# Kernel optimization log

Measured on AMD Instinct MI355X. Metric: run time of the kernel, lower is better.

## Reference

```python
import jax, jax.numpy as jnp
import numpy as np

B, T, C = 16, 1024, 512
K = 25          # decomp kernel_size
NW = 4          # num_wavelets
SEQ_LEN = T
EPS = 1e-5


def causal_ma(x, k):
    # causal moving average over time with replicate left-pad; x: [B,T,C]
    xp = jnp.pad(x, ((0, 0), (k - 1, 0), (0, 0)), mode='edge')
    cs = jnp.cumsum(xp, axis=1)
    cs0 = jnp.concatenate([jnp.zeros_like(cs[:, :1]), cs], axis=1)
    return (cs0[:, k:] - cs0[:, :-k]) / k


def dwconv3(x, w, b):
    # depthwise conv1d, kernel 3, replicate padding; x: [B,T,C], w: [C,3], b: [C]
    xp = jnp.pad(x, ((0, 0), (1, 1), (0, 0)), mode='edge')
    return xp[:, :-2] * w[:, 0] + xp[:, 1:-1] * w[:, 1] + xp[:, 2:] * w[:, 2] + b


def setup_inputs() -> dict:
    key = jax.random.key(0)
    ks = jax.random.split(key, 12)
    s = 0.02
    return {
        'x': jax.random.normal(ks[0], (B, T, C), dtype=jnp.float32),
        'trend_conv_w': jax.random.normal(ks[1], (C, 3), jnp.float32) * s,
        'trend_conv_b': jnp.zeros((C,), jnp.float32),
        'spike_conv_w': jax.random.normal(ks[2], (C, 3), jnp.float32) * s,
        'spike_conv_b': jnp.zeros((C,), jnp.float32),
        'slope_conv_w': jax.random.normal(ks[3], (C, 3), jnp.float32) * s,
        'slope_conv_b': jnp.zeros((C,), jnp.float32),
        'cheby_coeffs': jax.random.normal(ks[4], (C, C, 4), jnp.float32) * (1.0 / np.sqrt(C * 4)),
        'hyper_w1': jax.random.normal(ks[5], (2 * C, C), jnp.float32) * s,
        'hyper_b1': jnp.zeros((C,), jnp.float32),
        'hyper_w2': jax.random.normal(ks[6], (C, NW * 2), jnp.float32) * s,
        'hyper_b2': jnp.zeros((NW * 2,), jnp.float32),
        'amp_w': jax.random.normal(ks[7], (C, C), jnp.float32) * s,
        'amp_b': jnp.zeros((C,), jnp.float32),
        'wavelet_w': jax.random.normal(ks[8], (NW, C, C), jnp.float32) * (1.0 / np.sqrt(C)),
        'ln_gamma': jnp.ones((C,), jnp.float32),
        'ln_beta': jnp.zeros((C,), jnp.float32),
    }


def reference(x, trend_conv_w, trend_conv_b, spike_conv_w, spike_conv_b,
              slope_conv_w, slope_conv_b, cheby_coeffs,
              hyper_w1, hyper_b1, hyper_w2, hyper_b2,
              amp_w, amp_b, wavelet_w, ln_gamma, ln_beta):
    # --- causal frequency decomposition ---
    trend_part = causal_ma(x, K)              # [B,T,C]
    spike_part = x - trend_part

    # --- depthwise local convs ---
    trend_ctx = dwconv3(trend_part, trend_conv_w, trend_conv_b)
    spike_ctx = dwconv3(spike_part, spike_conv_w, spike_conv_b)

    # --- ChebyKAN on trend (degree 3) ---
    xt = jnp.tanh(trend_ctx)
    basis = jnp.stack([jnp.ones_like(xt), xt, 2 * xt * xt - 1,
                       xt * (4 * xt * xt - 3)], axis=-1)      # [B,T,C,4]
    trend_out = jnp.einsum('btcd,cod->bto', basis, cheby_coeffs)

    # --- hypernetwork for wavelet params ---
    slope = dwconv3(trend_part, slope_conv_w, slope_conv_b)
    slope_pool = slope.mean(axis=1)            # mean over time -> [B,C]
    value_pool = trend_part.mean(axis=1)       # [B,C]
    h = jnp.concatenate([slope_pool, value_pool], axis=-1)
    h = jax.nn.silu(h @ hyper_w1 + hyper_b1)
    params = (h @ hyper_w2 + hyper_b2).reshape(-1, 1, NW, 2)
    dyn_a = jax.nn.softplus(params[..., 0]) + 0.01          # [B,1,NW]
    dyn_b = jax.nn.sigmoid(params[..., 1]) * SEQ_LEN        # [B,1,NW]

    # --- adaptive wavelet KAN on spike ---
    pos = jnp.arange(T, dtype=x.dtype)[None, :, None]       # [1,T,1]
    z = (pos - dyn_b) / dyn_a                               # [B,T,NW]
    psi = (1.0 - z * z) * jnp.exp(-0.5 * z * z)             # Ricker wavelet
    spike_out = jnp.einsum('btw,btc,wco->bto', psi, spike_ctx, wavelet_w)

    # --- amplitude gate, residual, LayerNorm (dropout = identity in eval) ---
    amp_scale = jax.nn.sigmoid(trend_out @ amp_w + amp_b) * 2.0
    out = trend_out + spike_out * amp_scale
    y = out + x
    mu = y.mean(axis=-1, keepdims=True)
    var = ((y - mu) ** 2).mean(axis=-1, keepdims=True)
    return (y - mu) * jax.lax.rsqrt(var + EPS) * ln_gamma + ln_beta
```

## Files before the change

### kernel.cpp

```cpp
#include <hip/hip_runtime.h>
#include <hip/hip_bf16.h>
#include <math.h>

typedef __hip_bfloat16 bf16;
typedef __attribute__((ext_vector_type(8))) short s8v;
typedef __attribute__((ext_vector_type(4))) float f4v;

#define B_   16
#define T_   1024
#define C_   512
#define M_   (B_*T_)
#define NW_  4
#define KWIN 25
#define TCHUNK 16
#define NCHUNK (T_/TCHUNK)

__device__ __forceinline__ float b2f(bf16 v){ return __bfloat162float(v); }
__device__ __forceinline__ bf16  f2b(float v){ return __float2bfloat16(v); }

__device__ __forceinline__ float ftanh(float x){
    float e = __expf(2.f * x);
    return 1.f - 2.f * __builtin_amdgcn_rcpf(e + 1.f);
}
__device__ __forceinline__ float fsig(float x){
    return __builtin_amdgcn_rcpf(1.f + __expf(-x));
}

__device__ __forceinline__ void gload16(const bf16* g, bf16* l) {
    __builtin_amdgcn_global_load_lds(
        (const __attribute__((address_space(1))) void*)g,
        (__attribute__((address_space(3))) void*)l, 16, 0, 0);
}

__global__ __launch_bounds__(256) void repack_t_kernel(
    const float* __restrict__ wav, const float* __restrict__ ampw,
    bf16* __restrict__ WWT, bf16* __restrict__ AWT)
{
    __shared__ float tile[32][33];
    const int z = blockIdx.z;
    const int ct = blockIdx.x * 32, ot = blockIdx.y * 32;
    const int tx = threadIdx.x & 31, ty = threadIdx.x >> 5;
    const float* src = (z < 4) ? wav + (size_t)z * 262144 : ampw;
    #pragma unroll
    for (int r = 0; r < 32; r += 8)
        tile[ty + r][tx] = src[(size_t)(ct + ty + r) * 512 + ot + tx];
    __syncthreads();
    #pragma unroll
    for (int r = 0; r < 32; r += 8) {
        int o = ot + ty + r, c = ct + tx;
        bf16 v = f2b(tile[tx][ty + r]);
        if (z < 4) WWT[(size_t)o * 2048 + z * 512 + c] = v;
        else       AWT[(size_t)o * 512 + c] = v;
    }
}

__global__ __launch_bounds__(256) void repack_cct_kernel(
    const float* __restrict__ cheby,
    bf16* __restrict__ CCT)
{
    __shared__ float t1[32][33], t2[32][33], t3[32][33];
    const int ct = blockIdx.x * 32, ot = blockIdx.y * 32;
    const int tx = threadIdx.x & 31, ty = threadIdx.x >> 5;
    #pragma unroll
    for (int r = 0; r < 32; r += 8) {
        float4 w = *(const float4*)&cheby[(size_t)(ct + ty + r) * 2048 + (size_t)(ot + tx) * 4];
        t1[ty + r][tx] = w.y - 3.f * w.w;
        t2[ty + r][tx] = 2.f * w.z;
        t3[ty + r][tx] = 4.f * w.w;
    }
    __syncthreads();
    #pragma unroll
    for (int r = 0; r < 32; r += 8) {
        int o = ot + ty + r, c = ct + tx;
        size_t base = (size_t)o * 1536 + c;
        CCT[base]        = f2b(t1[tx][ty + r]);
        CCT[base + 512]  = f2b(t2[tx][ty + r]);
        CCT[base + 1024] = f2b(t3[tx][ty + r]);
    }
}

__global__ __launch_bounds__(256) void bias0_kernel(
    const float* __restrict__ cheby, float* __restrict__ bias0)
{
    __shared__ float red[8][33];
    const int tx = threadIdx.x & 31, ty = threadIdx.x >> 5;
    const int o = blockIdx.x * 32 + tx;
    float s = 0.f;
    for (int c = ty; c < 512; c += 8) {
        const float* p = &cheby[(size_t)c * 2048 + (size_t)o * 4];
        s += p[0] - p[2];
    }
    red[ty][tx] = s;
    __syncthreads();
    if (ty == 0) {
        float t = 0.f;
        #pragma unroll
        for (int q = 0; q < 8; ++q) t += red[q][tx];
        bias0[o] = t;
    }
}

__global__ __launch_bounds__(256) void transpose_w1_kernel(
    const float* __restrict__ w1, float* __restrict__ w1t)
{
    __shared__ float tile[32][33];
    const int bo = blockIdx.x, bj = blockIdx.y;
    const int tx = threadIdx.x & 31, ty = threadIdx.x >> 5;
    #pragma unroll
    for (int r = 0; r < 32; r += 8)
        tile[ty + r][tx] = w1[(size_t)(bj * 32 + ty + r) * 512 + bo * 32 + tx];
    __syncthreads();
    #pragma unroll
    for (int r = 0; r < 32; r += 8)
        w1t[(size_t)(bo * 32 + ty + r) * 1024 + bj * 32 + tx] = tile[tx][ty + r];
}

__global__ __launch_bounds__(256) void decomp_kernel(
    const float* __restrict__ x,
    const float* __restrict__ tcw, const float* __restrict__ tcb,
    const float* __restrict__ scw, const float* __restrict__ scb,
    const float* __restrict__ lcw, const float* __restrict__ lcb,
    bf16* __restrict__ xt,
    bf16* __restrict__ sctx,
    float* __restrict__ slope_part, float* __restrict__ value_part)
{
    const int c     = threadIdx.x * 2;
    const int chunk = blockIdx.x;
    const int b     = blockIdx.y;
    const int t0    = chunk * TCHUNK;
    const float* xb = x + (size_t)b * T_ * C_ + c;

    float w0t[2], w1t_[2], w2t[2], bt[2], w0s[2], w1s[2], w2s[2], bs[2], w0l[2], w1l[2], w2l[2], bl[2];
    #pragma unroll
    for (int e = 0; e < 2; ++e) {
        w0t[e]=tcw[(c+e)*3+0]; w1t_[e]=tcw[(c+e)*3+1]; w2t[e]=tcw[(c+e)*3+2]; bt[e]=tcb[c+e];
        w0s[e]=scw[(c+e)*3+0]; w1s[e]=scw[(c+e)*3+1]; w2s[e]=scw[(c+e)*3+2]; bs[e]=scb[c+e];
        w0l[e]=lcw[(c+e)*3+0]; w1l[e]=lcw[(c+e)*3+1]; w2l[e]=lcw[(c+e)*3+2]; bl[e]=lcb[c+e];
    }

    const float inv = 1.f / KWIN;
    float S0 = 0.f, S1 = 0.f;
    float trm[2], tr0[2], xm[2], x0v[2], sAcc[2] = {0.f,0.f}, vAcc[2] = {0.f,0.f};

    auto BODY = [&](int t, float2 an, float2 dn, bool adv) {
        float trp[2], xp[2];
        if (adv) {
            S0 += an.x - dn.x; S1 += an.y - dn.y;
            trp[0] = S0 * inv; trp[1] = S1 * inv;
            xp[0] = an.x; xp[1] = an.y;
        } else {
            trp[0] = tr0[0]; trp[1] = tr0[1];
            xp[0] = x0v[0];  xp[1] = x0v[1];
        }
        union { bf16 h[2]; unsigned u; } u1, usc;
        #pragma unroll
        for (int e = 0; e < 2; ++e) {
            float tctx = w0t[e]*trm[e] + w1t_[e]*tr0[e] + w2t[e]*trp[e] + bt[e];
            float sm = xm[e]-trm[e], s0 = x0v[e]-tr0[e], sp = xp[e]-trp[e];
            float sv = w0s[e]*sm + w1s[e]*s0 + w2s[e]*sp + bs[e];
            float sl = w0l[e]*trm[e] + w1l[e]*tr0[e] + w2l[e]*trp[e] + bl[e];
            sAcc[e] += sl; vAcc[e] += tr0[e];
            u1.h[e] = f2b(ftanh(tctx)); usc.h[e] = f2b(sv);
            trm[e] = tr0[e]; tr0[e] = trp[e]; xm[e] = x0v[e]; x0v[e] = xp[e];
        }
        size_t m = (size_t)b * T_ + t;
        *(unsigned*)&xt[m * C_ + c]   = u1.u;
        *(unsigned*)&sctx[m * C_ + c] = usc.u;
    };

    if (chunk >= 2 && chunk <= NCHUNK - 2) {
        const float* p = xb + (size_t)(t0 - KWIN) * C_;
        #pragma unroll
        for (int i = 0; i < KWIN; ++i) {
            float2 v = *(const float2*)(p + (size_t)i * C_);
            S0 += v.x; S1 += v.y;
        }
        trm[0] = S0 * inv; trm[1] = S1 * inv;
        float2 a = *(const float2*)(p + (size_t)KWIN * C_);
        float2 d = *(const float2*)p;
        S0 += a.x - d.x; S1 += a.y - d.y;
        tr0[0] = S0 * inv; tr0[1] = S1 * inv;
        float2 vm = *(const float2*)(p + (size_t)(KWIN - 1) * C_);
        xm[0] = vm.x; xm[1] = vm.y;
        x0v[0] = a.x; x0v[1] = a.y;

        #pragma unroll
        for (int tt = 0; tt < TCHUNK; ++tt) {
            float2 an = *(const float2*)(p + (size_t)(KWIN + 1 + tt) * C_);
            float2 dn = *(const float2*)(p + (size_t)(1 + tt) * C_);
            BODY(t0 + tt, an, dn, true);
        }
    } else {
        auto X = [&](int i) -> float2 {
            i = i < 0 ? 0 : (i > T_ - 1 ? T_ - 1 : i);
            return *(const float2*)&xb[(size_t)i * C_];
        };
        int j0 = (t0 > 0) ? (t0 - 1) : 0;
        #pragma unroll
        for (int i = j0 - (KWIN - 1); i <= j0; ++i) { float2 v = X(i); S0 += v.x; S1 += v.y; }
        trm[0] = S0 * inv; trm[1] = S1 * inv;
        if (t0 > 0) {
            float2 a = X(t0), d = X(t0 - KWIN);
            S0 += a.x - d.x; S1 += a.y - d.y;
            tr0[0] = S0 * inv; tr0[1] = S1 * inv;
        } else { tr0[0] = trm[0]; tr0[1] = trm[1]; }
        { float2 v = X(t0 - 1); xm[0] = v.x; xm[1] = v.y; }
        { float2 v = X(t0);     x0v[0] = v.x; x0v[1] = v.y; }

        #pragma unroll
        for (int tt = 0; tt < TCHUNK; ++tt) {
            int t = t0 + tt, tn = t + 1;
            bool adv = (tn <= T_ - 1);
            float2 an = make_float2(0.f, 0.f), dn = make_float2(0.f, 0.f);
            if (adv) { an = X(tn); dn = X(tn - KWIN); }
            BODY(t, an, dn, adv);
        }
    }
    int pidx = (chunk * B_ + b) * C_ + c;
    *(float2*)&slope_part[pidx] = make_float2(sAcc[0], sAcc[1]);
    *(float2*)&value_part[pidx] = make_float2(vAcc[0], vAcc[1]);
}

__global__ __launch_bounds__(256) void pool_kernel(
    const float* __restrict__ slope_part, const float* __restrict__ value_part,
    float* __restrict__ pc)
{
    int idx = blockIdx.x * 256 + threadIdx.x;
    int b = idx >> 10, j = idx & 1023;
    int c = j & 511;
    const float* src = (j < 512) ? slope_part : value_part;
    float s = 0.f;
    #pragma unroll 8
    for (int ch = 0; ch < NCHUNK; ++ch) s += src[(ch * B_ + b) * C_ + c];
    pc[idx] = s * (1.f / T_);
}

__global__ __launch_bounds__(256) void hyper1_kernel(
    const float* __restrict__ pc, const float* __restrict__ w1t,
    const float* __restrict__ b1, float* __restrict__ h)
{
    const int o = blockIdx.x, t = threadIdx.x;
    const float4 w = *(const float4*)&w1t[(size_t)o * 1024 + t * 4];
    float acc[16];
    #pragma unroll
    for (int b = 0; b < 16; ++b) {
        float4 p = *(const float4*)&pc[(size_t)b * 1024 + t * 4];
        acc[b] = w.x * p.x + w.y * p.y + w.z * p.z + w.w * p.w;
    }
    #pragma unroll
    for (int off = 32; off >= 1; off >>= 1)
        #pragma unroll
        for (int b = 0; b < 16; ++b) acc[b] += __shfl_down(acc[b], off);
    __shared__ float red[4][16];
    int lane = t & 63, wv = t >> 6;
    if (lane == 0)
        #pragma unroll
        for (int b = 0; b < 16; ++b) red[wv][b] = acc[b];
    __syncthreads();
    if (t < 16) {
        float s = red[0][t] + red[1][t] + red[2][t] + red[3][t] + b1[o];
        h[(size_t)t * 512 + o] = s / (1.f + expf(-s));
    }
}

__global__ __launch_bounds__(128) void hyper2_kernel(
    const float* __restrict__ h, const float* __restrict__ w2,
    const float* __restrict__ b2, float* __restrict__ dyn_a, float* __restrict__ dyn_b)
{
    __shared__ float pp[16][8];
    const int t = threadIdx.x, b = t >> 3, o = t & 7;
    float acc = b2[o];
    #pragma unroll 4
    for (int j = 0; j < 512; ++j) acc += h[(size_t)b * 512 + j] * w2[j * 8 + o];
    pp[b][o] = acc;
    __syncthreads();
    if (t < 64) {
        int bb = t >> 2, w = t & 3;
        float pa = pp[bb][2 * w], pb = pp[bb][2 * w + 1];
        float sp = fmaxf(pa, 0.f) + log1pf(expf(-fabsf(pa)));
        dyn_a[bb * NW_ + w] = sp + 0.01f;
        dyn_b[bb * NW_ + w] = (1.f / (1.f + expf(-pb))) * (float)T_;
    }
}

__global__ __launch_bounds__(256) void psi_kernel(
    const float* __restrict__ dyn_a, const float* __restrict__ dyn_b,
    float* __restrict__ psi)
{
    int idx = blockIdx.x * 256 + threadIdx.x;
    int w = idx & 3, m = idx >> 2;
    int b = m >> 10, t = m & 1023;
    float z = ((float)t - dyn_b[b * 4 + w]) / dyn_a[b * 4 + w];
    float z2 = z * z;
    psi[idx] = (1.f - z2) * expf(-0.5f * z2);
}

__global__ __launch_bounds__(512, 4) void gemm_big_kernel(
    const bf16* __restrict__ xt, const bf16* __restrict__ sctxg,
    const bf16* __restrict__ CCT, const bf16* __restrict__ WWT,
    const float* __restrict__ psi, const float* __restrict__ bias0,
    bf16* __restrict__ tout, bf16* __restrict__ sout)
{
    __shared__ bf16 lA[128 * 64];
    __shared__ bf16 lB[2][256 * 64];

    const int lin = blockIdx.x;
    const int swz = ((lin & 7) << 6) + (lin >> 3);
    const int mode = swz & 1;
    const int rem = swz >> 1;
    const int nb = rem & 1, mb = rem >> 1;
    const int m0 = mb << 7, n0 = nb << 8;

    const bf16* Ap = mode ? sctxg : xt;
    const bf16* Bp = mode ? WWT : CCT;
    bf16* Cp = mode ? sout : tout;
    const int K = mode ? 2048 : 1536;
    const int nK = K >> 6;

    const int tid = threadIdx.x;
    const int lane = tid & 63, wvi = tid >> 6;
    const int wr = wvi >> 2, wc = wvi & 3;
    const int r16 = lane & 15, g = lane >> 4;
    const int row8 = lane >> 3, sl8 = lane & 7;
    const int arow = tid >> 2, quad = tid & 3;

    float4 p4 = make_float4(0.f, 0.f, 0.f, 0.f);
    if (mode) p4 = *(const float4*)&psi[(size_t)(m0 + arow) * 4];

    const bf16* srcA = Ap + (size_t)(m0 + arow) * 512 + quad * 16;

    f4v acc[4][4];
    #pragma unroll
    for (int i = 0; i < 4; ++i)
        #pragma unroll
        for (int j = 0; j < 4; ++j) acc[i][j] = (f4v)0.f;

    s8v av0 = *(const s8v*)srcA;
    s8v av1 = *(const s8v*)(srcA + 8);
    #pragma unroll
    for (int c2 = 0; c2 < 4; ++c2) {
        int rb = c2 * 8 + wvi;
        int r = rb * 8 + row8;
        int ls = sl8 ^ (r & 7);
        gload16(Bp + (size_t)(n0 + r) * K + ls * 8, &lB[0][rb * 512]);
    }
    asm volatile("s_waitcnt vmcnt(4)" ::: "memory");

    for (int kt = 0; kt < nK; ++kt) {
        const int wsel = kt >> 3;
        const float sc = wsel == 0 ? p4.x : wsel == 1 ? p4.y : wsel == 2 ? p4.z : p4.w;

        #pragma unroll
        for (int j2 = 0; j2 < 2; ++j2) {
            s8v a = j2 ? av1 : av0;
            s8v ov;
            if (mode == 0) {
                if (wsel == 0) ov = a;
                else {
                    #pragma unroll
                    for (int e = 0; e < 8; ++e) {
                        float v = b2f(((const bf16*)&a)[e]);
                        float vv = v * v;
                        ((bf16*)&ov)[e] = f2b(wsel == 1 ? vv : vv * v);
                    }
                }
            } else {
                #pragma unroll
                for (int e = 0; e < 8; ++e)
                    ((bf16*)&ov)[e] = f2b(b2f(((const bf16*)&a)[e]) * sc);
            }
            int q = quad * 2 + j2;
            *(s8v*)&lA[arow * 64 + ((q ^ (arow & 7)) << 3)] = ov;
        }

        const int ktn = (kt + 1 < nK) ? kt + 1 : kt;
        const int kOffn = (ktn << 6) & 511;
        av0 = *(const s8v*)(srcA + kOffn);
        av1 = *(const s8v*)(srcA + kOffn + 8);

        {
            const int k0n = ktn << 6;
            bf16* dstB = lB[(kt + 1) & 1];
            #pragma unroll
            for (int c2 = 0; c2 < 4; ++c2) {
                int rb = c2 * 8 + wvi;
                int r = rb * 8 + row8;
                int ls = sl8 ^ (r & 7);
                gload16(Bp + (size_t)(n0 + r) * K + k0n + ls * 8, dstB + rb * 512);
            }
        }

        asm volatile("s_waitcnt vmcnt(4) lgkmcnt(0)" ::: "memory");
        asm volatile("s_barrier" ::: "memory");
        __builtin_amdgcn_sched_barrier(0);

        const bf16* lBc = lB[kt & 1];
        #pragma unroll
        for (int ks = 0; ks < 2; ++ks) {
            s8v afr[4], bfr[4];
            #pragma unroll
            for (int i = 0; i < 4; ++i) {
                int ar = wr * 64 + i * 16 + r16;
                afr[i] = *(const s8v*)((const char*)lA + ar * 128 + (((ks * 4 + g) ^ (ar & 7)) << 4));
            }
            #pragma unroll
            for (int j = 0; j < 4; ++j) {
                int br = wc * 64 + j * 16 + r16;
                bfr[j] = *(const s8v*)((const char*)lBc + br * 128 + (((ks * 4 + g) ^ (br & 7)) << 4));
            }
            #pragma unroll
            for (int i = 0; i < 4; ++i)
                #pragma unroll
                for (int j = 0; j < 4; ++j)
                    acc[i][j] = __builtin_amdgcn_mfma_f32_16x16x32_bf16(afr[i], bfr[j], acc[i][j], 0, 0, 0);
        }

        asm volatile("s_barrier" ::: "memory");
    }

    asm volatile("s_waitcnt vmcnt(0)" ::: "memory");

    #pragma unroll
    for (int i = 0; i < 4; ++i)
        #pragma unroll
        for (int j = 0; j < 4; ++j) {
            int cc = n0 + wc * 64 + j * 16 + r16;
            float bb = (mode == 0) ? bias0[cc] : 0.f;
            #pragma unroll
            for (int r = 0; r < 4; ++r) {
                int rr = m0 + wr * 64 + i * 16 + g * 4 + r;
                Cp[(size_t)rr * 512 + cc] = f2b(acc[i][j][r] + bb);
            }
        }
}

__global__ __launch_bounds__(512, 2) void amp_ln_kernel(
    const bf16* __restrict__ tout, const bf16* __restrict__ sout,
    const bf16* __restrict__ AWT,  const float* __restrict__ ampb,
    const float* __restrict__ x,   const float* __restrict__ gamma,
    const float* __restrict__ beta, float* __restrict__ out)
{
    __shared__ bf16 lA[64 * 64];
    __shared__ bf16 lB[512 * 64];
    __shared__ float red[64 * 16];

    const int m0 = blockIdx.x << 6;
    const int tid = threadIdx.x;
    const int lane = tid & 63, wvi = tid >> 6;
    const int wc = wvi;
    const int r16 = lane & 15, g = lane >> 4;
    const int row8 = lane >> 3, sl8 = lane & 7;

    f4v acc[4][4];
    #pragma unroll
    for (int i = 0; i < 4; ++i)
        #pragma unroll
        for (int j = 0; j < 4; ++j) acc[i][j] = (f4v)0.f;

    for (int kt = 0; kt < 8; ++kt) {
        const int k0 = kt << 6;
        {
            int r = (wvi << 3) + row8;
            int ls = sl8 ^ (r & 7);
            gload16(tout + (size_t)(m0 + r) * 512 + k0 + ls * 8, &lA[wvi * 512]);
        }
        #pragma unroll
        for (int c2 = 0; c2 < 8; ++c2) {
            int r = c2 * 64 + (wvi << 3) + row8;
            int ls = sl8 ^ (r & 7);
            gload16(AWT + (size_t)r * 512 + k0 + ls * 8, &lB[c2 * 4096 + wvi * 512]);
        }
        __syncthreads();
        #pragma unroll
        for (int ks = 0; ks < 2; ++ks) {
            s8v afr[4], bfr[4];
            #pragma unroll
            for (int i = 0; i < 4; ++i) {
                int ar = i * 16 + r16;
                afr[i] = *(const s8v*)((const char*)lA + ar * 128 + (((ks * 4 + g) ^ (ar & 7)) << 4));
            }
            #pragma unroll
            for (int j = 0; j < 4; ++j) {
                int br = wc * 64 + j * 16 + r16;
                bfr[j] = *(const s8v*)((const char*)lB + br * 128 + (((ks * 4 + g) ^ (br & 7)) << 4));
            }
            #pragma unroll
            for (int i = 0; i < 4; ++i)
                #pragma unroll
                for (int j = 0; j < 4; ++j)
                    acc[i][j] = __builtin_amdgcn_mfma_f32_16x16x32_bf16(afr[i], bfr[j], acc[i][j], 0, 0, 0);
        }
        __syncthreads();
    }

    float ab[4], gm[4], bt2[4];
    #pragma unroll
    for (int j = 0; j < 4; ++j) {
        int cc = wc * 64 + j * 16 + r16;
        ab[j] = ampb[cc]; gm[j] = gamma[cc]; bt2[j] = beta[cc];
    }
    f4v s4[4], q4[4];
    #pragma unroll
    for (int i = 0; i < 4; ++i) { s4[i] = (f4v)0.f; q4[i] = (f4v)0.f; }

    #pragma unroll
    for (int i = 0; i < 4; ++i)
        #pragma unroll
        for (int j = 0; j < 4; ++j) {
            int cc = wc * 64 + j * 16 + r16;
            #pragma unroll
            for (int r = 0; r < 4; ++r) {
                size_t rr = (size_t)(m0 + i * 16 + g * 4 + r);
                float amp = 2.f * fsig(acc[i][j][r] + ab[j]);
                float y = b2f(tout[rr * 512 + cc]) + b2f(sout[rr * 512 + cc]) * amp + x[rr * 512 + cc];
                acc[i][j][r] = y;
                s4[i][r] += y; q4[i][r] += y * y;
            }
        }

    #pragma unroll
    for (int off = 1; off < 16; off <<= 1)
        #pragma unroll
        for (int i = 0; i < 4; ++i)
            #pragma unroll
            for (int r = 0; r < 4; ++r) {
                s4[i][r] += __shfl_xor(s4[i][r], off);
                q4[i][r] += __shfl_xor(q4[i][r], off);
            }
    if (r16 == 0) {
        #pragma unroll
        for (int i = 0; i < 4; ++i)
            #pragma unroll
            for (int r = 0; r < 4; ++r) {
                int row = i * 16 + g * 4 + r;
                red[row * 16 + wvi * 2]     = s4[i][r];
                red[row * 16 + wvi * 2 + 1] = q4[i][r];
            }
    }
    __syncthreads();
    if (tid < 64) {
        float ts = 0.f, tq = 0.f;
        #pragma unroll
        for (int w = 0; w < 8; ++w) { ts += red[tid * 16 + w * 2]; tq += red[tid * 16 + w * 2 + 1]; }
        float mu = ts * (1.f / 512.f);
        float var = tq * (1.f / 512.f) - mu * mu;
        red[tid * 16]     = mu;
        red[tid * 16 + 1] = rsqrtf(var + 1e-5f);
    }
    __syncthreads();

    #pragma unroll
    for (int i = 0; i < 4; ++i)
        #pragma unroll
        for (int r = 0; r < 4; ++r) {
            int row = i * 16 + g * 4 + r;
            float mu = red[row * 16], rs = red[row * 16 + 1];
            size_t rr = (size_t)(m0 + row);
            #pragma unroll
            for (int j = 0; j < 4; ++j) {
                int cc = wc * 64 + j * 16 + r16;
                out[rr * 512 + cc] = (acc[i][j][r] - mu) * rs * gm[j] + bt2[j];
            }
        }
}

extern "C" void kernel_launch(void* const* d_in, const int* in_sizes, int n_in,
                              void* d_out, int out_size, void* d_ws, size_t ws_size,
                              hipStream_t stream)
{
    const float* x     = (const float*)d_in[0];
    const float* tcw   = (const float*)d_in[1];
    const float* tcb   = (const float*)d_in[2];
    const float* scw   = (const float*)d_in[3];
    const float* scb   = (const float*)d_in[4];
    const float* lcw   = (const float*)d_in[5];
    const float* lcb   = (const float*)d_in[6];
    const float* cheby = (const float*)d_in[7];
    const float* hw1   = (const float*)d_in[8];
    const float* hb1   = (const float*)d_in[9];
    const float* hw2   = (const float*)d_in[10];
    const float* hb2   = (const float*)d_in[11];
    const float* ampw  = (const float*)d_in[12];
    const float* ampb  = (const float*)d_in[13];
    const float* wav   = (const float*)d_in[14];
    const float* lng   = (const float*)d_in[15];
    const float* lnb   = (const float*)d_in[16];
    float* out = (float*)d_out;

    char* ws = (char*)d_ws;
    size_t off = 0;
    auto alloc = [&](size_t bytes) -> char* {
        char* p = ws + off;
        off += (bytes + 255) & ~(size_t)255;
        return p;
    };
    bf16*  xt         = (bf16*)alloc((size_t)M_ * 512 * 2);
    bf16*  sctx       = (bf16*)alloc((size_t)M_ * 512 * 2);
    bf16*  tout       = (bf16*)alloc((size_t)M_ * 512 * 2);
    bf16*  sout       = (bf16*)alloc((size_t)M_ * 512 * 2);
    bf16*  CCT        = (bf16*)alloc((size_t)512 * 1536 * 2);
    bf16*  WWT        = (bf16*)alloc((size_t)512 * 2048 * 2);
    bf16*  AWT        = (bf16*)alloc((size_t)512 * 512 * 2);
    float* W1T        = (float*)alloc((size_t)512 * 1024 * 4);
    float* bias0      = (float*)alloc(512 * 4);
    float* slope_part = (float*)alloc((size_t)NCHUNK * B_ * C_ * 4);
    float* value_part = (float*)alloc((size_t)NCHUNK * B_ * C_ * 4);
    float* pc         = (float*)alloc(B_ * 1024 * 4);
    float* hbuf       = (float*)alloc(B_ * C_ * 4);
    float* dyn_a      = (float*)alloc(B_ * NW_ * 4);
    float* dyn_b      = (float*)alloc(B_ * NW_ * 4);
    float* psi        = (float*)alloc((size_t)M_ * NW_ * 4);

    repack_t_kernel<<<dim3(16, 16, 5), 256, 0, stream>>>(wav, ampw, WWT, AWT);
    repack_cct_kernel<<<dim3(16, 16), 256, 0, stream>>>(cheby, CCT);
    bias0_kernel<<<16, 256, 0, stream>>>(cheby, bias0);
    transpose_w1_kernel<<<dim3(16, 32), 256, 0, stream>>>(hw1, W1T);
    decomp_kernel<<<dim3(NCHUNK, B_), 256, 0, stream>>>(x, tcw, tcb, scw, scb, lcw, lcb,
                                                        xt, sctx, slope_part, value_part);
    pool_kernel<<<64, 256, 0, stream>>>(slope_part, value_part, pc);
    hyper1_kernel<<<512, 256, 0, stream>>>(pc, W1T, hb1, hbuf);
    hyper2_kernel<<<1, 128, 0, stream>>>(hbuf, hw2, hb2, dyn_a, dyn_b);
    psi_kernel<<<256, 256, 0, stream>>>(dyn_a, dyn_b, psi);
    gemm_big_kernel<<<512, 512, 0, stream>>>(xt, sctx, CCT, WWT, psi, bias0, tout, sout);
    amp_ln_kernel<<<256, 512, 0, stream>>>(tout, sout, AWT, ampb, x, lng, lnb, out);
}
```

Baseline: 198.7 us.

## Fuse prep kernels, inline psi into GEMM, skip negligible wavelet segments

Merges the four weight-repack and transpose kernels into one prep kernel, and moves the bias0 reduction into the pool kernel as per-tile partial sums. The psi kernel is removed: the GEMM now computes Ricker wavelet values directly from dyn_a and dyn_b. Each block of the spike GEMM takes a block-wide max of |psi| per wavelet and skips both the LDS staging and the MFMA work for K-segments whose max is below 1e-6. This targets launch overhead and wasted matrix work on wavelets that are effectively zero for a tile. In exchange it adds shared-memory atomics and extra barriers, and it relies on a small-value threshold.

```diff
diff --git a/kernel.cpp b/kernel.cpp
--- a/kernel.cpp
+++ b/kernel.cpp
@@ -32,87 +32,68 @@
         (__attribute__((address_space(3))) void*)l, 16, 0, 0);
 }
 
-__global__ __launch_bounds__(256) void repack_t_kernel(
-    const float* __restrict__ wav, const float* __restrict__ ampw,
-    bf16* __restrict__ WWT, bf16* __restrict__ AWT)
-{
-    __shared__ float tile[32][33];
-    const int z = blockIdx.z;
-    const int ct = blockIdx.x * 32, ot = blockIdx.y * 32;
+__global__ __launch_bounds__(256) void prep_kernel(
+    const float* __restrict__ wav,  const float* __restrict__ ampw,
+    const float* __restrict__ cheby, const float* __restrict__ w1,
+    bf16* __restrict__ WWT, bf16* __restrict__ AWT, bf16* __restrict__ CCT,
+    float* __restrict__ bias0_part, float* __restrict__ w1t)
+{
+    __shared__ float t0[32][33], t1[32][33], t2[32][33], t3[32][33];
+    const int blk = blockIdx.x;
     const int tx = threadIdx.x & 31, ty = threadIdx.x >> 5;
-    const float* src = (z < 4) ? wav + (size_t)z * 262144 : ampw;
-    #pragma unroll
-    for (int r = 0; r < 32; r += 8)
-        tile[ty + r][tx] = src[(size_t)(ct + ty + r) * 512 + ot + tx];
-    __syncthreads();
-    #pragma unroll
-    for (int r = 0; r < 32; r += 8) {
-        int o = ot + ty + r, c = ct + tx;
-        bf16 v = f2b(tile[tx][ty + r]);
-        if (z < 4) WWT[(size_t)o * 2048 + z * 512 + c] = v;
-        else       AWT[(size_t)o * 512 + c] = v;
-    }
-}
-
-__global__ __launch_bounds__(256) void repack_cct_kernel(
-    const float* __restrict__ cheby,
-    bf16* __restrict__ CCT)
-{
-    __shared__ float t1[32][33], t2[32][33], t3[32][33];
-    const int ct = blockIdx.x * 32, ot = blockIdx.y * 32;
-    const int tx = threadIdx.x & 31, ty = threadIdx.x >> 5;
-    #pragma unroll
-    for (int r = 0; r < 32; r += 8) {
-        float4 w = *(const float4*)&cheby[(size_t)(ct + ty + r) * 2048 + (size_t)(ot + tx) * 4];
-        t1[ty + r][tx] = w.y - 3.f * w.w;
-        t2[ty + r][tx] = 2.f * w.z;
-        t3[ty + r][tx] = 4.f * w.w;
-    }
-    __syncthreads();
-    #pragma unroll
-    for (int r = 0; r < 32; r += 8) {
-        int o = ot + ty + r, c = ct + tx;
-        size_t base = (size_t)o * 1536 + c;
-        CCT[base]        = f2b(t1[tx][ty + r]);
-        CCT[base + 512]  = f2b(t2[tx][ty + r]);
-        CCT[base + 1024] = f2b(t3[tx][ty + r]);
-    }
-}
-
-__global__ __launch_bounds__(256) void bias0_kernel(
-    const float* __restrict__ cheby, float* __restrict__ bias0)
-{
-    __shared__ float red[8][33];
-    const int tx = threadIdx.x & 31, ty = threadIdx.x >> 5;
-    const int o = blockIdx.x * 32 + tx;
-    float s = 0.f;
-    for (int c = ty; c < 512; c += 8) {
-        const float* p = &cheby[(size_t)c * 2048 + (size_t)o * 4];
-        s += p[0] - p[2];
-    }
-    red[ty][tx] = s;
-    __syncthreads();
-    if (ty == 0) {
-        float t = 0.f;
-        #pragma unroll
-        for (int q = 0; q < 8; ++q) t += red[q][tx];
-        bias0[o] = t;
-    }
-}
-
-__global__ __launch_bounds__(256) void transpose_w1_kernel(
-    const float* __restrict__ w1, float* __restrict__ w1t)
-{
-    __shared__ float tile[32][33];
-    const int bo = blockIdx.x, bj = blockIdx.y;
-    const int tx = threadIdx.x & 31, ty = threadIdx.x >> 5;
-    #pragma unroll
-    for (int r = 0; r < 32; r += 8)
-        tile[ty + r][tx] = w1[(size_t)(bj * 32 + ty + r) * 512 + bo * 32 + tx];
-    __syncthreads();
-    #pragma unroll
-    for (int r = 0; r < 32; r += 8)
-        w1t[(size_t)(bo * 32 + ty + r) * 1024 + bj * 32 + tx] = tile[tx][ty + r];
+
+    if (blk < 1280) {
+        const int z = blk >> 8, rem = blk & 255;
+        const int ct = (rem & 15) * 32, ot = (rem >> 4) * 32;
+        const float* src = (z < 4) ? wav + (size_t)z * 262144 : ampw;
+        #pragma unroll
+        for (int r = 0; r < 32; r += 8)
+            t0[ty + r][tx] = src[(size_t)(ct + ty + r) * 512 + ot + tx];
+        __syncthreads();
+        #pragma unroll
+        for (int r = 0; r < 32; r += 8) {
+            int o = ot + ty + r, c = ct + tx;
+            bf16 v = f2b(t0[tx][ty + r]);
+            if (z < 4) WWT[(size_t)o * 2048 + z * 512 + c] = v;
+            else       AWT[(size_t)o * 512 + c] = v;
+        }
+    } else if (blk < 1536) {
+        const int rem = blk - 1280;
+        const int ct = (rem & 15) * 32, ot = (rem >> 4) * 32;
+        #pragma unroll
+        for (int r = 0; r < 32; r += 8) {
+            float4 w = *(const float4*)&cheby[(size_t)(ct + ty + r) * 2048 + (size_t)(ot + tx) * 4];
+            t0[ty + r][tx] = w.x - w.z;
+            t1[ty + r][tx] = w.y - 3.f * w.w;
+            t2[ty + r][tx] = 2.f * w.z;
+            t3[ty + r][tx] = 4.f * w.w;
+        }
+        __syncthreads();
+        #pragma unroll
+        for (int r = 0; r < 32; r += 8) {
+            int o = ot + ty + r, c = ct + tx;
+            size_t base = (size_t)o * 1536 + c;
+            CCT[base]        = f2b(t1[tx][ty + r]);
+            CCT[base + 512]  = f2b(t2[tx][ty + r]);
+            CCT[base + 1024] = f2b(t3[tx][ty + r]);
+        }
+        if (threadIdx.x < 32) {
+            float s = 0.f;
+            #pragma unroll
+            for (int cr = 0; cr < 32; ++cr) s += t0[cr][threadIdx.x];
+            bias0_part[(size_t)(rem & 15) * 512 + ot + threadIdx.x] = s;
+        }
+    } else {
+        const int rem = blk - 1536;
+        const int bo = rem & 15, bj = rem >> 4;
+        #pragma unroll
+        for (int r = 0; r < 32; r += 8)
+            t0[ty + r][tx] = w1[(size_t)(bj * 32 + ty + r) * 512 + bo * 32 + tx];
+        __syncthreads();
+        #pragma unroll
+        for (int r = 0; r < 32; r += 8)
+            w1t[(size_t)(bo * 32 + ty + r) * 1024 + bj * 32 + tx] = t0[tx][ty + r];
+    }
 }
 
 __global__ __launch_bounds__(256) void decomp_kernel(
@@ -120,8 +101,7 @@
     const float* __restrict__ tcw, const float* __restrict__ tcb,
     const float* __restrict__ scw, const float* __restrict__ scb,
     const float* __restrict__ lcw, const float* __restrict__ lcb,
-    bf16* __restrict__ xt,
-    bf16* __restrict__ sctx,
+    bf16* __restrict__ xt, bf16* __restrict__ sctx,
     float* __restrict__ slope_part, float* __restrict__ value_part)
 {
     const int c     = threadIdx.x * 2;
@@ -223,7 +203,8 @@
 
 __global__ __launch_bounds__(256) void pool_kernel(
     const float* __restrict__ slope_part, const float* __restrict__ value_part,
-    float* __restrict__ pc)
+    const float* __restrict__ bias0_part,
+    float* __restrict__ pc, float* __restrict__ bias0)
 {
     int idx = blockIdx.x * 256 + threadIdx.x;
     int b = idx >> 10, j = idx & 1023;
@@ -233,6 +214,12 @@
     #pragma unroll 8
     for (int ch = 0; ch < NCHUNK; ++ch) s += src[(ch * B_ + b) * C_ + c];
     pc[idx] = s * (1.f / T_);
+    if (idx < 512) {
+        float t = 0.f;
+        #pragma unroll
+        for (int i = 0; i < 16; ++i) t += bias0_part[(size_t)i * 512 + idx];
+        bias0[idx] = t;
+    }
 }
 
 __global__ __launch_bounds__(256) void hyper1_kernel(
@@ -283,22 +270,11 @@
     }
 }
 
-__global__ __launch_bounds__(256) void psi_kernel(
-    const float* __restrict__ dyn_a, const float* __restrict__ dyn_b,
-    float* __restrict__ psi)
-{
-    int idx = blockIdx.x * 256 + threadIdx.x;
-    int w = idx & 3, m = idx >> 2;
-    int b = m >> 10, t = m & 1023;
-    float z = ((float)t - dyn_b[b * 4 + w]) / dyn_a[b * 4 + w];
-    float z2 = z * z;
-    psi[idx] = (1.f - z2) * expf(-0.5f * z2);
-}
-
 __global__ __launch_bounds__(512, 4) void gemm_big_kernel(
     const bf16* __restrict__ xt, const bf16* __restrict__ sctxg,
     const bf16* __restrict__ CCT, const bf16* __restrict__ WWT,
-    const float* __restrict__ psi, const float* __restrict__ bias0,
+    const float* __restrict__ dyn_a, const float* __restrict__ dyn_b,
+    const float* __restrict__ bias0,
     bf16* __restrict__ tout, bf16* __restrict__ sout)
 {
     __shared__ bf16 lA[128 * 64];
@@ -325,7 +301,38 @@
     const int arow = tid >> 2, quad = tid & 3;
 
     float4 p4 = make_float4(0.f, 0.f, 0.f, 0.f);
-    if (mode) p4 = *(const float4*)&psi[(size_t)(m0 + arow) * 4];
+    bool alive[4] = {true, true, true, true};
+    if (mode) {
+        int* wmaxsh = (int*)lA;
+        if (tid < 4) wmaxsh[tid] = 0;
+        __syncthreads();
+        const int bIdx = m0 >> 10;
+        const float tpos = (float)((m0 + arow) & 1023);
+        float pv[4], am[4];
+        #pragma unroll
+        for (int w = 0; w < 4; ++w) {
+            float z = (tpos - dyn_b[bIdx * 4 + w]) / dyn_a[bIdx * 4 + w];
+            float z2 = z * z;
+            pv[w] = (1.f - z2) * __expf(-0.5f * z2);
+            am[w] = fabsf(pv[w]);
+        }
+        p4 = make_float4(pv[0], pv[1], pv[2], pv[3]);
+        #pragma unroll
+        for (int off = 32; off >= 1; off >>= 1)
+            #pragma unroll
+            for (int w = 0; w < 4; ++w) am[w] = fmaxf(am[w], __shfl_xor(am[w], off));
+        if (lane == 0) {
+            #pragma unroll
+            for (int w = 0; w < 4; ++w) atomicMax(&wmaxsh[w], __float_as_int(am[w]));
+        }
+        __syncthreads();
+        #pragma unroll
+        for (int w = 0; w < 4; ++w) {
+            float f = __int_as_float(__builtin_amdgcn_readfirstlane(wmaxsh[w]));
+            alive[w] = f > 1e-6f;
+        }
+        __syncthreads();
+    }
 
     const bf16* srcA = Ap + (size_t)(m0 + arow) * 512 + quad * 16;
 
@@ -348,29 +355,32 @@
 
     for (int kt = 0; kt < nK; ++kt) {
         const int wsel = kt >> 3;
+        const bool aliveSeg = alive[wsel];
         const float sc = wsel == 0 ? p4.x : wsel == 1 ? p4.y : wsel == 2 ? p4.z : p4.w;
 
-        #pragma unroll
-        for (int j2 = 0; j2 < 2; ++j2) {
-            s8v a = j2 ? av1 : av0;
-            s8v ov;
-            if (mode == 0) {
-                if (wsel == 0) ov = a;
-                else {
+        if (aliveSeg) {
+            #pragma unroll
+            for (int j2 = 0; j2 < 2; ++j2) {
+                s8v a = j2 ? av1 : av0;
+                s8v ov;
+                if (mode == 0) {
+                    if (wsel == 0) ov = a;
+                    else {
+                        #pragma unroll
+                        for (int e = 0; e < 8; ++e) {
+                            float v = b2f(((const bf16*)&a)[e]);
+                            float vv = v * v;
+                            ((bf16*)&ov)[e] = f2b(wsel == 1 ? vv : vv * v);
+                        }
+                    }
+                } else {
                     #pragma unroll
-                    for (int e = 0; e < 8; ++e) {
-                        float v = b2f(((const bf16*)&a)[e]);
-                        float vv = v * v;
-                        ((bf16*)&ov)[e] = f2b(wsel == 1 ? vv : vv * v);
-                    }
+                    for (int e = 0; e < 8; ++e)
+                        ((bf16*)&ov)[e] = f2b(b2f(((const bf16*)&a)[e]) * sc);
                 }
-            } else {
-                #pragma unroll
-                for (int e = 0; e < 8; ++e)
-                    ((bf16*)&ov)[e] = f2b(b2f(((const bf16*)&a)[e]) * sc);
-            }
-            int q = quad * 2 + j2;
-            *(s8v*)&lA[arow * 64 + ((q ^ (arow & 7)) << 3)] = ov;
+                int q = quad * 2 + j2;
+                *(s8v*)&lA[arow * 64 + ((q ^ (arow & 7)) << 3)] = ov;
+            }
         }
 
         const int ktn = (kt + 1 < nK) ? kt + 1 : kt;
@@ -394,25 +404,27 @@
         asm volatile("s_barrier" ::: "memory");
         __builtin_amdgcn_sched_barrier(0);
 
-        const bf16* lBc = lB[kt & 1];
-        #pragma unroll
-        for (int ks = 0; ks < 2; ++ks) {
-            s8v afr[4], bfr[4];
-            #pragma unroll
-            for (int i = 0; i < 4; ++i) {
-                int ar = wr * 64 + i * 16 + r16;
-                afr[i] = *(const s8v*)((const char*)lA + ar * 128 + (((ks * 4 + g) ^ (ar & 7)) << 4));
-            }
-            #pragma unroll
-            for (int j = 0; j < 4; ++j) {
-                int br = wc * 64 + j * 16 + r16;
-                bfr[j] = *(const s8v*)((const char*)lBc + br * 128 + (((ks * 4 + g) ^ (br & 7)) << 4));
-            }
-            #pragma unroll
-            for (int i = 0; i < 4; ++i)
+        if (aliveSeg) {
+            const bf16* lBc = lB[kt & 1];
+            #pragma unroll
+            for (int ks = 0; ks < 2; ++ks) {
+                s8v afr[4], bfr[4];
                 #pragma unroll
-                for (int j = 0; j < 4; ++j)
-                    acc[i][j] = __builtin_amdgcn_mfma_f32_16x16x32_bf16(afr[i], bfr[j], acc[i][j], 0, 0, 0);
+                for (int i = 0; i < 4; ++i) {
+                    int ar = wr * 64 + i * 16 + r16;
+                    afr[i] = *(const s8v*)((const char*)lA + ar * 128 + (((ks * 4 + g) ^ (ar & 7)) << 4));
+                }
+                #pragma unroll
+                for (int j = 0; j < 4; ++j) {
+                    int br = wc * 64 + j * 16 + r16;
+                    bfr[j] = *(const s8v*)((const char*)lBc + br * 128 + (((ks * 4 + g) ^ (br & 7)) << 4));
+                }
+                #pragma unroll
+                for (int i = 0; i < 4; ++i)
+                    #pragma unroll
+                    for (int j = 0; j < 4; ++j)
+                        acc[i][j] = __builtin_amdgcn_mfma_f32_16x16x32_bf16(afr[i], bfr[j], acc[i][j], 0, 0, 0);
+            }
         }
 
         asm volatile("s_barrier" ::: "memory");
@@ -602,6 +614,7 @@
     bf16*  WWT        = (bf16*)alloc((size_t)512 * 2048 * 2);
     bf16*  AWT        = (bf16*)alloc((size_t)512 * 512 * 2);
     float* W1T        = (float*)alloc((size_t)512 * 1024 * 4);
+    float* bias0_part = (float*)alloc((size_t)16 * 512 * 4);
     float* bias0      = (float*)alloc(512 * 4);
     float* slope_part = (float*)alloc((size_t)NCHUNK * B_ * C_ * 4);
     float* value_part = (float*)alloc((size_t)NCHUNK * B_ * C_ * 4);
@@ -609,18 +622,13 @@
     float* hbuf       = (float*)alloc(B_ * C_ * 4);
     float* dyn_a      = (float*)alloc(B_ * NW_ * 4);
     float* dyn_b      = (float*)alloc(B_ * NW_ * 4);
-    float* psi        = (float*)alloc((size_t)M_ * NW_ * 4);
-
-    repack_t_kernel<<<dim3(16, 16, 5), 256, 0, stream>>>(wav, ampw, WWT, AWT);
-    repack_cct_kernel<<<dim3(16, 16), 256, 0, stream>>>(cheby, CCT);
-    bias0_kernel<<<16, 256, 0, stream>>>(cheby, bias0);
-    transpose_w1_kernel<<<dim3(16, 32), 256, 0, stream>>>(hw1, W1T);
+
+    prep_kernel<<<2048, 256, 0, stream>>>(wav, ampw, cheby, hw1, WWT, AWT, CCT, bias0_part, W1T);
     decomp_kernel<<<dim3(NCHUNK, B_), 256, 0, stream>>>(x, tcw, tcb, scw, scb, lcw, lcb,
                                                         xt, sctx, slope_part, value_part);
-    pool_kernel<<<64, 256, 0, stream>>>(slope_part, value_part, pc);
+    pool_kernel<<<64, 256, 0, stream>>>(slope_part, value_part, bias0_part, pc, bias0);
     hyper1_kernel<<<512, 256, 0, stream>>>(pc, W1T, hb1, hbuf);
     hyper2_kernel<<<1, 128, 0, stream>>>(hbuf, hw2, hb2, dyn_a, dyn_b);
-    psi_kernel<<<256, 256, 0, stream>>>(dyn_a, dyn_b, psi);
-    gemm_big_kernel<<<512, 512, 0, stream>>>(xt, sctx, CCT, WWT, psi, bias0, tout, sout);
+    gemm_big_kernel<<<512, 512, 0, stream>>>(xt, sctx, CCT, WWT, dyn_a, dyn_b, bias0, tout, sout);
     amp_ln_kernel<<<256, 512, 0, stream>>>(tout, sout, AWT, ampb, x, lng, lnb, out);
 }
```

Result: faster. 172.4 us (-13.2%).
